# Optimization experiments

Hardware: AMD Instinct MI355X
Metric: run time of the kernel (lower is better)

## Reference

```python
import jax, jax.numpy as jnp
import numpy as np

KERNEL = 10   # kernel_size (asserted == 10 in the original)
HEADS = 4
BN_SCALE = 1.0 / np.sqrt(1.0 + 1e-5)  # eval-mode BatchNorm1d (running mean 0, var 1, affine 1/0)


def get_dct_matrix(N):
    k = np.arange(N)[:, None].astype(np.float64)
    i = np.arange(N)[None, :].astype(np.float64)
    w = np.full((N, 1), np.sqrt(2.0 / N))
    w[0, 0] = np.sqrt(1.0 / N)
    dct_m = w * np.cos(np.pi * (i + 0.5) * k / N)
    idct_m = np.linalg.inv(dct_m)
    return dct_m.astype(np.float32), idct_m.astype(np.float32)


def conv1d(x, w):  # x [B,C,L], w [O,I,K], valid, no bias
    return jax.lax.conv_general_dilated(x, w, (1,), 'VALID',
                                        dimension_numbers=('NCH', 'OIH', 'NCH'))


def conv_stack(x, w1, w2):  # Conv1d(k=6) -> ReLU -> Conv1d(k=5) -> ReLU
    return jax.nn.relu(conv1d(jax.nn.relu(conv1d(x, w1)), w2))


# vmap over the 4 heads' weights -> [H,B,D,L]
heads_conv = jax.vmap(conv_stack, in_axes=(None, 0, 0))


def _forward(src, cq1, cq2, ck1, ck2, lw, lb, giw, gia, gib, gbw, gba, gbb,
             gow, goa, gob, dct_n, output_n, input_n):
    bs, in_feat = src.shape[0], src.shape[2]
    src = src[:, :input_n]                                   # [B,50,48]
    src_key = jnp.swapaxes(src, 1, 2)[:, :, :input_n - output_n]  # [B,48,25]
    src_query = jnp.swapaxes(src, 1, 2)[:, :, -KERNEL:]           # [B,48,10]

    dct_np, idct_np = get_dct_matrix(KERNEL + output_n)
    dct_m = jnp.asarray(dct_np)
    idct_m = jnp.asarray(idct_np)

    vn = input_n - KERNEL - output_n + 1  # 16 overlapping value windows
    vl = KERNEL + output_n                # window length 35
    idx = np.arange(vl)[None, :] + np.arange(vn)[:, None]    # [16,35]
    windows = src[:, idx]                                    # [B,16,35,48]
    # DCT per window then flatten per-joint coeffs: [B,16,48*dct_n]
    val = jnp.einsum('dv,bnvf->bndf', dct_m[:dct_n], windows)
    src_value = jnp.swapaxes(val, 2, 3).reshape(bs, vn, -1)  # [B,16,480]

    key_h = heads_conv(src_key / 1000.0, ck1, ck2)           # [H,B,512,16]
    query_h = heads_conv(src_query / 1000.0, cq1, cq2)       # [H,B,512,1]

    # sum-normalized (non-softmax) attention
    score = jnp.einsum('hbdq,hbdk->hbqk', query_h, key_h) + 1e-15  # [H,B,1,16]
    att_w = score / jnp.sum(score, axis=3, keepdims=True)
    dct_att = jnp.einsum('hbk,bkf->hbf', att_w[:, :, 0], src_value)  # [H,B,480]
    dct_att = dct_att.reshape(HEADS, bs, in_feat, dct_n)
    att_cat = jnp.transpose(dct_att, (1, 0, 2, 3)).reshape(bs, HEADS * in_feat, dct_n)
    # Linear over the concatenated head/joint axis: [B,48,dct_n]
    att_lin = jnp.einsum('bmd,nm->bnd', att_cat, lw) + lb[None, :, None]

    # last kernel_size frames + last frame repeated output_n times
    gather_idx = np.concatenate([np.arange(input_n - KERNEL, input_n),
                                 np.full(output_n, input_n - 1)])
    input_gcn = src[:, gather_idx]                           # [B,35,48]
    dct_in = jnp.einsum('dv,bvf->bfd', dct_m[:dct_n], input_gcn)  # [B,48,10]
    dct_in = jnp.concatenate([dct_in, att_lin], axis=-1)     # [B,48,20]

    # GCN (Mao et al. style): learnable adjacency [48,48], eval-mode BN, tanh
    def gc(h, a, w, b):
        return jnp.einsum('nm,bmf->bnf', a, h @ w) + b

    y = jnp.tanh(gc(dct_in, gia, giw, gib) * BN_SCALE)       # [B,48,512]
    for s in range(gbw.shape[0]):
        r = y
        for j in range(2):
            y = jnp.tanh(gc(y, gba[s, j], gbw[s, j], gbb[s, j]) * BN_SCALE)
        y = y + r
    dct_out = gc(y, goa, gow, gob) + dct_in                  # [B,48,20]

    out_gcn = jnp.einsum('vd,bnd->bvn', idct_m[:, :dct_n], dct_out[:, :, :dct_n])  # [B,35,48]
    return out_gcn[:, :, None, :]                            # [B,35,itera=1,48]


def setup_inputs() -> dict:
    key = jax.random.key(0)
    ks = jax.random.split(key, 16)
    bs, in_feat, d_model, dct_n = 256, 48, 512, 10
    s = 0.05
    return {
        'src': jax.random.normal(ks[0], (bs, 50, in_feat), jnp.float32) * 1000.0,
        'convQ_w1': jax.random.normal(ks[1], (HEADS, d_model, in_feat, 6), jnp.float32) * s,
        'convQ_w2': jax.random.normal(ks[2], (HEADS, d_model, d_model, 5), jnp.float32) * s,
        'convK_w1': jax.random.normal(ks[3], (HEADS, d_model, in_feat, 6), jnp.float32) * s,
        'convK_w2': jax.random.normal(ks[4], (HEADS, d_model, d_model, 5), jnp.float32) * s,
        'linear_w': jax.random.normal(ks[5], (in_feat, HEADS * in_feat), jnp.float32) * s,
        'linear_b': jax.random.normal(ks[6], (in_feat,), jnp.float32) * s,
        'gc_in_w': jax.random.normal(ks[7], (2 * dct_n, d_model), jnp.float32) * s,
        'gc_in_att': jax.random.normal(ks[8], (in_feat, in_feat), jnp.float32) * s,
        'gc_in_b': jax.random.normal(ks[9], (d_model,), jnp.float32) * s,
        'gcb_w': jax.random.normal(ks[10], (2, 2, d_model, d_model), jnp.float32) * s,
        'gcb_att': jax.random.normal(ks[11], (2, 2, in_feat, in_feat), jnp.float32) * s,
        'gcb_b': jax.random.normal(ks[12], (2, 2, d_model), jnp.float32) * s,
        'gc_out_w': jax.random.normal(ks[13], (d_model, 2 * dct_n), jnp.float32) * s,
        'gc_out_att': jax.random.normal(ks[14], (in_feat, in_feat), jnp.float32) * s,
        'gc_out_b': jax.random.normal(ks[15], (2 * dct_n,), jnp.float32) * s,
        'dct_n': 10, 'output_n': 25, 'input_n': 50, 'itera': 1,
    }


def reference(src, convQ_w1, convQ_w2, convK_w1, convK_w2, linear_w, linear_b,
              gc_in_w, gc_in_att, gc_in_b, gcb_w, gcb_att, gcb_b,
              gc_out_w, gc_out_att, gc_out_b, dct_n, output_n, input_n, itera):
    # itera=1 path only (itera>1 in the original references undefined attrs)
    return _forward(src, convQ_w1, convQ_w2, convK_w1, convK_w2, linear_w, linear_b,
                    gc_in_w, gc_in_att, gc_in_b, gcb_w, gcb_att, gcb_b,
                    gc_out_w, gc_out_att, gc_out_b, dct_n, output_n, input_n)
```

## Files before the change

### kernel.cpp

```cpp
#include <hip/hip_runtime.h>
#include <math.h>

static constexpr float BN_SCALE_F = 0.9999950000374997f;

typedef __bf16 bf16;
typedef bf16 bf16x8 __attribute__((ext_vector_type(8)));
typedef bf16 bf16x4 __attribute__((ext_vector_type(4)));
typedef float floatx4 __attribute__((ext_vector_type(4)));

#define GLOBAL_AS __attribute__((address_space(1)))
#define LDS_AS __attribute__((address_space(3)))

enum { BM_SRC = 0, BM_R1K = 1, BM_PLAIN = 3 };

__device__ __forceinline__ float tanh_fast(float x) {
    const float e = __expf(2.f * x);
    return 1.f - 2.f / (e + 1.f);
}

__device__ __forceinline__ void d_trw1(int id, const float* w, bf16* wt) {
    if (id < 4 * 512 * 320) {
        int ho = id / 320, c = id % 320;
        float v = (c < 288) ? w[(long)ho * 288 + (c % 48) * 6 + (c / 48)] * 1e-3f : 0.f;
        wt[id] = (bf16)v;
    }
}
__global__ __launch_bounds__(256) void k_prep(
    const float* __restrict__ src, const float* __restrict__ cq1,
    const float* __restrict__ ck1, const float* __restrict__ cq2,
    const float* __restrict__ ck2, const float* __restrict__ gbw,
    const float* __restrict__ giw, const float* __restrict__ gow,
    const float* __restrict__ gba, float* __restrict__ dct10,
    bf16* __restrict__ srcbf, bf16* __restrict__ w1tq, bf16* __restrict__ w1tk,
    bf16* __restrict__ w2tq, bf16* __restrict__ w2tk, bf16* __restrict__ gbwt,
    bf16* __restrict__ giwP, bf16* __restrict__ gowT, bf16* __restrict__ gbaP) {
    __shared__ float lds[4160];
    int bb = blockIdx.x;
    const int t = threadIdx.x;
    if (bb < 2) {
        int id = bb * 256 + t;
        if (id < 350) {
            int k = id / 35, i = id % 35;
            double w = (k == 0) ? sqrt(1.0 / 35.0) : sqrt(2.0 / 35.0);
            dct10[id] = (float)(w * cos(3.14159265358979323846 * (i + 0.5) * k / 35.0));
        }
        return;
    }
    bb -= 2;
    if (bb < 2401) {
        int id = bb * 256 + t;
        if (id < 614656) srcbf[id] = (bf16)(id < 614400 ? src[id] : 0.f);
        return;
    }
    bb -= 2401;
    if (bb < 2560) { d_trw1(bb * 256 + t, cq1, w1tq); return; }
    bb -= 2560;
    if (bb < 2560) { d_trw1(bb * 256 + t, ck1, w1tk); return; }
    bb -= 2560;
    if (bb < 4096) {
        const bool isQ = bb < 2048;
        const int ho = isQ ? bb : bb - 2048;
        const float* wrow = (isQ ? cq2 : ck2) + (long)ho * 2560;
        bf16* orow = (isQ ? w2tq : w2tk) + (long)ho * 2560;
        for (int j = t; j < 2560; j += 256) lds[j] = wrow[j];
        __syncthreads();
        for (int c = t; c < 2560; c += 256) {
            const int k = c >> 9, ii = c & 511;
            orow[c] = (bf16)lds[ii * 5 + k];
        }
        return;
    }
    bb -= 4096;
    if (bb < 256) {
        const int s = bb >> 6, tile = bb & 63;
        const int tr = tile >> 3, tc = tile & 7;
        const float* in = gbw + (long)s * 262144;
        bf16* o = gbwt + (long)s * 262144;
#pragma unroll
        for (int r = 0; r < 16; ++r) {
            const int kl = (t >> 6) * 16 + r, ml = t & 63;
            lds[kl * 65 + ml] = in[(long)(tr * 64 + kl) * 512 + tc * 64 + ml];
        }
        __syncthreads();
#pragma unroll
        for (int r = 0; r < 16; ++r) {
            const int ml = (t >> 6) * 16 + r, kl = t & 63;
            o[(long)(tc * 64 + ml) * 512 + tr * 64 + kl] = (bf16)lds[kl * 65 + ml];
        }
        return;
    }
    bb -= 256;
    if (bb < 128) {
        int id = bb * 256 + t;
        if (id < 512 * 64) {
            int f = id >> 6, k = id & 63;
            giwP[id] = (bf16)(k < 20 ? giw[k * 512 + f] : 0.f);
        }
        return;
    }
    bb -= 128;
    if (bb < 64) {
        int id = bb * 256 + t;
        int d = id >> 9, k = id & 511;
        gowT[id] = (bf16)(d < 20 ? gow[k * 20 + d] : 0.f);
        return;
    }
    bb -= 64;
    {
        int id = bb * 256 + t;
        if (id < 12288) {
            int l = id / 3072, r = id % 3072, n = r >> 6, m = r & 63;
            gbaP[id] = (bf16)(m < 48 ? gba[l * 2304 + n * 48 + m] : 0.f);
        }
    }
}

struct GP {
    const bf16* A;
    const bf16* B;
    bf16* C;
    int NT;
    int toff;
    int nTiles;
    long aStr, bStr, cStr;
};
template <int BM1, int BM2>
__global__ __launch_bounds__(256) void mgemm2(GP p1, GP p2, const int splitX,
                                              const int M, const int K) {
    const bool first = (int)blockIdx.x < splitX;
    const GP p = first ? p1 : p2;
    const int bx = first ? (int)blockIdx.x : (int)blockIdx.x - splitX;
    if (bx >= p.nTiles) return;
    __shared__ bf16 As[128 * 64];
    __shared__ bf16 Bs[128 * 64];
    const int tid = threadIdx.x;
    const int wave = tid >> 6;
    const int lane = tid & 63;
    const int wm = (wave & 1) << 6;
    const int wn = (wave >> 1) << 6;
    const int m0 = blockIdx.y * 128;
    const int n0 = bx * 128;
    const bf16* A = p.A + (long)blockIdx.z * p.aStr;
    const bf16* B = p.B + (long)blockIdx.z * p.bStr;

    const int srow = lane >> 3;
    const int gch = (lane & 7) ^ srow;
    const bf16* aptr[4];
    const bf16* bptr[4];
#pragma unroll
    for (int i = 0; i < 4; ++i) {
        const int ar = wave * 32 + i * 8 + srow;
        aptr[i] = A + (long)(m0 + ar) * K + gch * 8;
        const int n = n0 + ar;
        long bbase;
        const bool isSrc = first ? (BM1 == BM_SRC) : (BM2 == BM_SRC);
        if (isSrc)
            bbase = (long)(n / p.NT) * 2400 + (long)((n % p.NT) + p.toff) * 48;
        else
            bbase = (long)n * K;
        bptr[i] = B + bbase + gch * 8;
    }
    const int ldsOff = wave * 32 * 64;

    floatx4 acc[4][4];
#pragma unroll
    for (int j = 0; j < 4; ++j)
#pragma unroll
        for (int i = 0; i < 4; ++i) acc[j][i] = (floatx4){0.f, 0.f, 0.f, 0.f};

    const int fr = lane & 15;
    const int fq = lane >> 4;
    const int fx = lane & 7;

    for (int k0 = 0; k0 < K; k0 += 64) {
#pragma unroll
        for (int i = 0; i < 4; ++i) {
            __builtin_amdgcn_global_load_lds(
                (const GLOBAL_AS void*)(aptr[i] + k0),
                (LDS_AS void*)(As + ldsOff + i * 512), 16, 0, 0);
            __builtin_amdgcn_global_load_lds(
                (const GLOBAL_AS void*)(bptr[i] + k0),
                (LDS_AS void*)(Bs + ldsOff + i * 512), 16, 0, 0);
        }
        __syncthreads();
#pragma unroll
        for (int kk = 0; kk < 2; ++kk) {
            bf16x8 af[4], bfr[4];
#pragma unroll
            for (int im = 0; im < 4; ++im)
                af[im] = *(const bf16x8*)(As + (wm + im * 16 + fr) * 64 +
                                          ((((kk << 2) + fq) ^ fx) << 3));
#pragma unroll
            for (int in = 0; in < 4; ++in)
                bfr[in] = *(const bf16x8*)(Bs + (wn + in * 16 + fr) * 64 +
                                           ((((kk << 2) + fq) ^ fx) << 3));
#pragma unroll
            for (int in = 0; in < 4; ++in)
#pragma unroll
                for (int im = 0; im < 4; ++im)
                    acc[in][im] = __builtin_amdgcn_mfma_f32_16x16x32_bf16(
                        af[im], bfr[in], acc[in][im], 0, 0, 0);
        }
        __syncthreads();
    }
#pragma unroll
    for (int in = 0; in < 4; ++in) {
        const long n = n0 + wn + in * 16 + fr;
#pragma unroll
        for (int im = 0; im < 4; ++im) {
            floatx4 v = acc[in][im];
            const long m = m0 + wm + im * 16 + (fq << 2);
            v.x = fmaxf(v.x, 0.f);
            v.y = fmaxf(v.y, 0.f);
            v.z = fmaxf(v.z, 0.f);
            v.w = fmaxf(v.w, 0.f);
            bf16* C = p.C + (long)blockIdx.z * p.cStr + n * M + m;
            bf16x4 ov;
            ov[0] = (bf16)v.x;
            ov[1] = (bf16)v.y;
            ov[2] = (bf16)v.z;
            ov[3] = (bf16)v.w;
            *(bf16x4*)C = ov;
        }
    }
}

__global__ __launch_bounds__(256) void k_conv2(
    const bf16* __restrict__ w2tk, const bf16* __restrict__ r1k,
    bf16* __restrict__ keyh, const bf16* __restrict__ w2tq,
    const bf16* __restrict__ r1q, bf16* __restrict__ qh) {
    const int M = 512, K = 2560;
    int bx, by, bz;
    const bf16 *A, *B;
    bf16* C;
    bool r1kMode;
    long aStr, bStr, cStr;
    {
        const int i = blockIdx.x;
        if (i < 512) {
            const int slot = i & 7;
            bz = slot & 3;
            const int half = slot >> 2;
            const int j = i >> 3;
            bx = half * 16 + (j & 15);
            by = j >> 4;
            A = w2tk; B = r1k; C = keyh; r1kMode = true;
            aStr = 512L * 2560; bStr = 2621440L; cStr = 2097152L;
        } else {
            const int j = i - 512;
            bx = j & 1;
            by = (j >> 1) & 3;
            bz = j >> 3;
            A = w2tq; B = r1q; C = qh; r1kMode = false;
            aStr = 512L * 2560; bStr = 655360L; cStr = 131072L;
        }
    }
    __shared__ bf16 As[128 * 64];
    __shared__ bf16 Bs[128 * 64];
    const int tid = threadIdx.x;
    const int wave = tid >> 6;
    const int lane = tid & 63;
    const int wm = (wave & 1) << 6;
    const int wn = (wave >> 1) << 6;
    const int m0 = by * 128;
    const int n0 = bx * 128;
    A += (long)bz * aStr;
    B += (long)bz * bStr;

    const int srow = lane >> 3;
    const int gch = (lane & 7) ^ srow;
    const bf16* aptr[4];
    const bf16* bptr[4];
#pragma unroll
    for (int i = 0; i < 4; ++i) {
        const int ar = wave * 32 + i * 8 + srow;
        aptr[i] = A + (long)(m0 + ar) * K + gch * 8;
        const int n = n0 + ar;
        const long bbase = r1kMode ? (long)((n >> 4) * 20 + (n & 15)) * 512
                                   : (long)n * K;
        bptr[i] = B + bbase + gch * 8;
    }
    const int ldsOff = wave * 32 * 64;

    floatx4 acc[4][4];
#pragma unroll
    for (int j = 0; j < 4; ++j)
#pragma unroll
        for (int i = 0; i < 4; ++i) acc[j][i] = (floatx4){0.f, 0.f, 0.f, 0.f};

    const int fr = lane & 15;
    const int fq = lane >> 4;
    const int fx = lane & 7;

    for (int k0 = 0; k0 < K; k0 += 64) {
#pragma unroll
        for (int i = 0; i < 4; ++i) {
            __builtin_amdgcn_global_load_lds(
                (const GLOBAL_AS void*)(aptr[i] + k0),
                (LDS_AS void*)(As + ldsOff + i * 512), 16, 0, 0);
            __builtin_amdgcn_global_load_lds(
                (const GLOBAL_AS void*)(bptr[i] + k0),
                (LDS_AS void*)(Bs + ldsOff + i * 512), 16, 0, 0);
        }
        __syncthreads();
#pragma unroll
        for (int kk = 0; kk < 2; ++kk) {
            bf16x8 af[4], bfr[4];
#pragma unroll
            for (int im = 0; im < 4; ++im)
                af[im] = *(const bf16x8*)(As + (wm + im * 16 + fr) * 64 +
                                          ((((kk << 2) + fq) ^ fx) << 3));
#pragma unroll
            for (int in = 0; in < 4; ++in)
                bfr[in] = *(const bf16x8*)(Bs + (wn + in * 16 + fr) * 64 +
                                           ((((kk << 2) + fq) ^ fx) << 3));
#pragma unroll
            for (int in = 0; in < 4; ++in)
#pragma unroll
                for (int im = 0; im < 4; ++im)
                    acc[in][im] = __builtin_amdgcn_mfma_f32_16x16x32_bf16(
                        af[im], bfr[in], acc[in][im], 0, 0, 0);
        }
        __syncthreads();
    }
#pragma unroll
    for (int in = 0; in < 4; ++in) {
        const long n = n0 + wn + in * 16 + fr;
#pragma unroll
        for (int im = 0; im < 4; ++im) {
            floatx4 v = acc[in][im];
            const long m = m0 + wm + im * 16 + (fq << 2);
            v.x = fmaxf(v.x, 0.f);
            v.y = fmaxf(v.y, 0.f);
            v.z = fmaxf(v.z, 0.f);
            v.w = fmaxf(v.w, 0.f);
            bf16* Cp = C + (long)bz * cStr + n * M + m;
            bf16x4 ov;
            ov[0] = (bf16)v.x;
            ov[1] = (bf16)v.y;
            ov[2] = (bf16)v.z;
            ov[3] = (bf16)v.w;
            *(bf16x4*)Cp = ov;
        }
    }
}

__global__ __launch_bounds__(512) void k_att(
    const bf16* __restrict__ qh, const bf16* __restrict__ keyh,
    const float* __restrict__ src, const float* __restrict__ dct10,
    const float* __restrict__ lw, const float* __restrict__ lb,
    const float* __restrict__ gia, float* __restrict__ dctin,
    bf16* __restrict__ z0) {
    const int b = blockIdx.x;
    const int t = threadIdx.x;
    __shared__ float BIG[9216];
    __shared__ float WD[2400];
    __shared__ float D[350];
    __shared__ float L[1920];
    __shared__ float dinS[960];
    __shared__ float sS[64];
    __shared__ float awS[64];

    {
        const int g = t >> 3, lane = t & 7;
        const int h = g >> 4, tt = g & 15;
        const bf16* q = qh + ((long)h * 256 + b) * 512 + lane * 64;
        const bf16* kr = keyh + (long)h * 2097152 + ((long)b * 16 + tt) * 512 + lane * 64;
        float p = 0.f;
#pragma unroll
        for (int i = 0; i < 8; ++i) {
            const bf16x8 qv = *(const bf16x8*)(q + i * 8);
            const bf16x8 kv = *(const bf16x8*)(kr + i * 8);
#pragma unroll
            for (int j = 0; j < 8; ++j) p = fmaf((float)qv[j], (float)kv[j], p);
        }
        p += __shfl_down(p, 4, 8);
        p += __shfl_down(p, 2, 8);
        p += __shfl_down(p, 1, 8);
        if (lane == 0) sS[g] = p + 1e-15f;
    }
    for (int i = t; i < 2400; i += 512) WD[i] = src[(long)b * 2400 + i];
    for (int i = t; i < 350; i += 512) D[i] = dct10[i];
    __syncthreads();
    if (t < 4) {
        float s = 0.f;
#pragma unroll
        for (int k = 0; k < 16; ++k) s += sS[t * 16 + k];
        const float inv = 1.f / s;
#pragma unroll
        for (int k = 0; k < 16; ++k) awS[t * 16 + k] = sS[t * 16 + k] * inv;
    }
    __syncthreads();
    if (t < 480) {
        const int f = t / 10, d = t % 10;
        float dreg[35];
#pragma unroll
        for (int v = 0; v < 35; ++v) dreg[v] = D[d * 35 + v];
#pragma unroll 2
        for (int n = 0; n < 16; ++n) {
            float acc = 0.f;
#pragma unroll
            for (int v = 0; v < 35; ++v)
                acc = fmaf(dreg[v], WD[(n + v) * 48 + f], acc);
            BIG[n * 480 + t] = acc;
        }
        float acc = 0.f;
#pragma unroll
        for (int v = 0; v < 10; ++v)
            acc = fmaf(dreg[v], WD[(40 + v) * 48 + f], acc);
        float cs = 0.f;
#pragma unroll
        for (int v = 10; v < 35; ++v) cs += dreg[v];
        acc = fmaf(cs, WD[49 * 48 + f], acc);
        dinS[f * 20 + d] = acc;
        dctin[(long)b * 960 + f * 20 + d] = acc;
    }
    __syncthreads();
    for (int p = 0; p < 4; ++p) {
        const int idx = t + p * 512;
        if (idx < 1920) {
            const int h = idx / 480, j = idx % 480;
            float acc = 0.f;
#pragma unroll
            for (int k = 0; k < 16; ++k)
                acc = fmaf(awS[h * 16 + k], BIG[k * 480 + j], acc);
            L[idx] = acc;
        }
    }
    __syncthreads();
    for (int i = t; i < 9216; i += 512) BIG[i] = lw[i];
    for (int i = t; i < 2304; i += 512) WD[i] = gia[i];
    __syncthreads();
    if (t < 480) {
        const int n = t / 10, d = t % 10;
        float acc = lb[n];
#pragma unroll
        for (int h = 0; h < 4; ++h)
#pragma unroll
            for (int f = 0; f < 48; ++f)
                acc = fmaf(BIG[n * 192 + h * 48 + f], L[h * 480 + f * 10 + d], acc);
        dinS[n * 20 + 10 + d] = acc;
        dctin[(long)b * 960 + n * 20 + 10 + d] = acc;
    }
    __syncthreads();
    for (int p = 0; p < 2; ++p) {
        const int idx = t + p * 512;
        if (idx < 960) {
            const int n = idx / 20, d = idx % 20;
            float acc = 0.f;
#pragma unroll
            for (int m = 0; m < 48; ++m)
                acc = fmaf(WD[n * 48 + m], dinS[m * 20 + d], acc);
            z0[((long)b * 48 + n) * 64 + d] = (bf16)acc;
        }
    }
    for (int i = t; i < 2112; i += 512) {
        const int n = i / 44, c = 20 + i % 44;
        z0[((long)b * 48 + n) * 64 + c] = (bf16)0.f;
    }
}

template <bool TOUT>
__device__ __forceinline__ void gcn_matmul2(
    const bf16* __restrict__ zSrc, const bf16* __restrict__ Bg, const int K,
    const float* __restrict__ bias, const bf16* __restrict__ resT,
    bf16* __restrict__ outS, const int wave, const int lane) {
    const int fr = lane & 15, fq = lane >> 4;
    const int f0 = wave * 32;
    floatx4 acc[3][2];
#pragma unroll
    for (int it = 0; it < 3; ++it)
#pragma unroll
        for (int jt = 0; jt < 2; ++jt) acc[it][jt] = (floatx4){0.f, 0.f, 0.f, 0.f};
    const bf16* bp0 = Bg + (long)(f0 + fr) * K + fq * 8;
    const bf16* bp1 = bp0 + 16 * (long)K;
    bf16x8 a0 = *(const bf16x8*)(bp0);
    bf16x8 a1 = *(const bf16x8*)(bp1);
    bf16x8 b0 = *(const bf16x8*)(bp0 + 32);
    bf16x8 b1 = *(const bf16x8*)(bp1 + 32);
    for (int k0 = 0; k0 < K; k0 += 64) {
        bf16x8 p0 = a0, p1 = a1, q0 = b0, q1 = b1;
        if (k0 + 64 < K) {
            p0 = *(const bf16x8*)(bp0 + k0 + 64);
            p1 = *(const bf16x8*)(bp1 + k0 + 64);
            q0 = *(const bf16x8*)(bp0 + k0 + 96);
            q1 = *(const bf16x8*)(bp1 + k0 + 96);
        }
        bf16x8 af[3];
#pragma unroll
        for (int it = 0; it < 3; ++it)
            af[it] = *(const bf16x8*)(zSrc + (it * 16 + fr) * 520 + k0 + fq * 8);
#pragma unroll
        for (int it = 0; it < 3; ++it) {
            acc[it][0] = __builtin_amdgcn_mfma_f32_16x16x32_bf16(af[it], a0,
                                                                acc[it][0], 0, 0, 0);
            acc[it][1] = __builtin_amdgcn_mfma_f32_16x16x32_bf16(af[it], a1,
                                                                acc[it][1], 0, 0, 0);
        }
#pragma unroll
        for (int it = 0; it < 3; ++it)
            af[it] = *(const bf16x8*)(zSrc + (it * 16 + fr) * 520 + k0 + 32 + fq * 8);
#pragma unroll
        for (int it = 0; it < 3; ++it) {
            acc[it][0] = __builtin_amdgcn_mfma_f32_16x16x32_bf16(af[it], b0,
                                                                acc[it][0], 0, 0, 0);
            acc[it][1] = __builtin_amdgcn_mfma_f32_16x16x32_bf16(af[it], b1,
                                                                acc[it][1], 0, 0, 0);
        }
        a0 = p0; a1 = p1; b0 = q0; b1 = q1;
    }
#pragma unroll
    for (int jt = 0; jt < 2; ++jt) {
        const int f = f0 + jt * 16 + fr;
        const float bv = bias[f];
#pragma unroll
        for (int it = 0; it < 3; ++it)
#pragma unroll
            for (int r = 0; r < 4; ++r) {
                const int irow = it * 16 + fq * 4 + r;
                float v = tanh_fast((acc[it][jt][r] + bv) * BN_SCALE_F);
                if (resT) v += (float)resT[f * 48 + irow];
                if (TOUT)
                    outS[f * 48 + irow] = (bf16)v;
                else
                    outS[irow * 520 + f] = (bf16)v;
            }
    }
}

__device__ __forceinline__ void gcn_attmul2(const bf16* __restrict__ gA,
                                            const bf16* __restrict__ YinT,
                                            bf16* __restrict__ zOut,
                                            const int wave, const int lane) {
    const int fr = lane & 15, fq = lane >> 4;
    const int f0 = wave * 32;
    floatx4 acc[3][2];
#pragma unroll
    for (int it = 0; it < 3; ++it)
#pragma unroll
        for (int jt = 0; jt < 2; ++jt) acc[it][jt] = (floatx4){0.f, 0.f, 0.f, 0.f};
    bf16x8 af0[3], af1[3], bv0[2], bv1[2];
#pragma unroll
    for (int it = 0; it < 3; ++it) {
        af0[it] = *(const bf16x8*)(gA + (it * 16 + fr) * 64 + fq * 8);
        af1[it] = *(const bf16x8*)(gA + (it * 16 + fr) * 64 + 32 + fq * 8);
    }
#pragma unroll
    for (int jt = 0; jt < 2; ++jt) {
        const int f = f0 + jt * 16 + fr;
        bv0[jt] = *(const bf16x8*)(YinT + f * 48 + fq * 8);
        bv1[jt] = *(const bf16x8*)(YinT + f * 48 + 32 + fq * 8);
    }
#pragma unroll
    for (int it = 0; it < 3; ++it)
#pragma unroll
        for (int jt = 0; jt < 2; ++jt) {
            acc[it][jt] = __builtin_amdgcn_mfma_f32_16x16x32_bf16(af0[it], bv0[jt],
                                                                 acc[it][jt], 0, 0, 0);
            acc[it][jt] = __builtin_amdgcn_mfma_f32_16x16x32_bf16(af1[it], bv1[jt],
                                                                 acc[it][jt], 0, 0, 0);
        }
#pragma unroll
    for (int jt = 0; jt < 2; ++jt) {
        const int f = f0 + jt * 16 + fr;
#pragma unroll
        for (int it = 0; it < 3; ++it)
#pragma unroll
            for (int r = 0; r < 4; ++r)
                zOut[(it * 16 + fq * 4 + r) * 520 + f] = (bf16)acc[it][jt][r];
    }
}

__global__ __launch_bounds__(1024) void k_gcn(
    const bf16* __restrict__ z0, const bf16* __restrict__ giwP,
    const float* __restrict__ gib, const bf16* __restrict__ gbwt,
    const bf16* __restrict__ gbaP, const float* __restrict__ gbb,
    const float* __restrict__ goa, const bf16* __restrict__ gowT,
    const float* __restrict__ gob, const float* __restrict__ dctin,
    const float* __restrict__ dct10, float* __restrict__ out) {
    const int b = blockIdx.x;
    const int t = threadIdx.x;
    const int wave = t >> 6, lane = t & 63;
    __shared__ __align__(16) bf16 yaS[24976];
    __shared__ __align__(16) bf16 ybS[24592];
    __shared__ __align__(16) bf16 zS[48 * 520];

    if (t < 384) {
        const int r = t >> 3, c = t & 7;
        *(bf16x8*)(zS + r * 520 + c * 8) =
            *(const bf16x8*)(z0 + ((long)b * 48 + r) * 64 + c * 8);
    } else if (t < 400) {
        yaS[24576 + (t - 384)] = (bf16)0.f;
    } else if (t < 416) {
        ybS[24576 + (t - 400)] = (bf16)0.f;
    }
    __syncthreads();
    gcn_matmul2<true>(zS, giwP, 64, gib, nullptr, yaS, wave, lane);
    __syncthreads();

#pragma unroll
    for (int l = 0; l < 4; ++l) {
        const bf16* YinT = (l == 0 || l == 3) ? yaS : ybS;
        gcn_attmul2(gbaP + l * 3072, YinT, zS, wave, lane);
        __syncthreads();
        const bf16* Res = (l == 1) ? yaS : (l == 3 ? ybS : nullptr);
        if (l < 3)
            gcn_matmul2<true>(zS, gbwt + (long)l * 262144, 512, gbb + l * 512,
                              Res, (l < 2) ? ybS : yaS, wave, lane);
        else
            gcn_matmul2<false>(zS, gbwt + 3L * 262144, 512, gbb + 3 * 512, Res,
                               yaS, wave, lane);
        __syncthreads();
    }
    float* T2 = (float*)ybS;
    float* dS = ((float*)ybS) + 960;
    float* goaS = ((float*)ybS) + 1920;
    float* Df = ((float*)ybS) + 4224;
    if (t < 384) {
        const int fr2 = lane & 15, fq2 = lane >> 4;
        const int it = wave >> 1, jt = wave & 1;
        floatx4 accT = (floatx4){0.f, 0.f, 0.f, 0.f};
        const bf16* ap = yaS + (it * 16 + fr2) * 520 + fq2 * 8;
        const bf16* gp = gowT + (long)(jt * 16 + fr2) * 512 + fq2 * 8;
        for (int k0 = 0; k0 < 512; k0 += 32) {
            const bf16x8 av = *(const bf16x8*)(ap + k0);
            const bf16x8 gv = *(const bf16x8*)(gp + k0);
            accT = __builtin_amdgcn_mfma_f32_16x16x32_bf16(av, gv, accT, 0, 0, 0);
        }
        const int d = jt * 16 + fr2;
        if (d < 20) {
#pragma unroll
            for (int r = 0; r < 4; ++r) {
                const int m = it * 16 + fq2 * 4 + r;
                T2[m * 20 + d] = accT[r];
            }
        }
    } else {
        for (int i = t - 384; i < 2304; i += 640) goaS[i] = goa[i];
        for (int i = t - 384; i < 350; i += 640) Df[i] = dct10[i];
    }
    __syncthreads();
    if (t < 960) {
        const int n = t / 20, d = t % 20;
        float acc = gob[d] + dctin[(long)b * 960 + t];
#pragma unroll
        for (int m = 0; m < 48; ++m)
            acc = fmaf(goaS[n * 48 + m], T2[m * 20 + d], acc);
        dS[t] = acc;
    }
    __syncthreads();
    for (int e = t; e < 1680; e += 1024) {
        const int v = e / 48, n = e % 48;
        float acc = 0.f;
#pragma unroll
        for (int d = 0; d < 10; ++d)
            acc = fmaf(Df[d * 35 + v], dS[n * 20 + d], acc);
        out[(long)b * 1680 + e] = acc;
    }
}

static constexpr size_t WS_DCT10 = 0;
static constexpr size_t WS_ATTW = 1536;
static constexpr size_t WS_QH = WS_ATTW + 65536;
static constexpr size_t WS_DCTIN = WS_QH + 2097152;
static constexpr size_t WS_DCTOUT = WS_DCTIN + 983040;
static constexpr size_t WS_SRCVAL = WS_DCTOUT + 983040;
static constexpr size_t WS_PAD0 = WS_SRCVAL + 7864320;
static constexpr size_t WS_GOWT = WS_PAD0;
static constexpr size_t WS_GBAP = WS_PAD0 + 32768;
static constexpr size_t WS_SRCBF = WS_PAD0 + 8388608;
static constexpr size_t WS_W1TQ = WS_SRCBF + 1229824;
static constexpr size_t WS_W1TK = WS_W1TQ + 1310720;
static constexpr size_t WS_W2TQ = WS_W1TK + 1310720;
static constexpr size_t WS_W2TK = WS_W2TQ + 10485760;
static constexpr size_t WS_GBWT = WS_W2TK + 10485760;
static constexpr size_t WS_R1K = WS_GBWT + 2097152;
static constexpr size_t WS_R1Q = WS_R1K + 20971520;
static constexpr size_t WS_T = WS_R1Q + 5242880;
static constexpr size_t WS_GIWP = WS_T + 50331648;
static constexpr size_t WS_KEYH = WS_T;
static constexpr size_t WS_Z0 = WS_T + 17825792;

extern "C" void kernel_launch(void* const* d_in, const int* in_sizes, int n_in,
                              void* d_out, int out_size, void* d_ws,
                              size_t ws_size, hipStream_t stream) {
    const float* src = (const float*)d_in[0];
    const float* cq1 = (const float*)d_in[1];
    const float* cq2 = (const float*)d_in[2];
    const float* ck1 = (const float*)d_in[3];
    const float* ck2 = (const float*)d_in[4];
    const float* lw = (const float*)d_in[5];
    const float* lb = (const float*)d_in[6];
    const float* giw = (const float*)d_in[7];
    const float* gia = (const float*)d_in[8];
    const float* gib = (const float*)d_in[9];
    const float* gbw = (const float*)d_in[10];
    const float* gba = (const float*)d_in[11];
    const float* gbb = (const float*)d_in[12];
    const float* gow = (const float*)d_in[13];
    const float* goa = (const float*)d_in[14];
    const float* gob = (const float*)d_in[15];
    float* out = (float*)d_out;
    char* ws = (char*)d_ws;

    float* dct10 = (float*)(ws + WS_DCT10);
    bf16* qh = (bf16*)(ws + WS_QH);
    float* dctin = (float*)(ws + WS_DCTIN);
    bf16* keyh = (bf16*)(ws + WS_KEYH);
    bf16* srcbf = (bf16*)(ws + WS_SRCBF);
    bf16* w1tq = (bf16*)(ws + WS_W1TQ);
    bf16* w1tk = (bf16*)(ws + WS_W1TK);
    bf16* w2tq = (bf16*)(ws + WS_W2TQ);
    bf16* w2tk = (bf16*)(ws + WS_W2TK);
    bf16* gbwt = (bf16*)(ws + WS_GBWT);
    bf16* r1k = (bf16*)(ws + WS_R1K);
    bf16* r1q = (bf16*)(ws + WS_R1Q);
    bf16* giwP = (bf16*)(ws + WS_GIWP);
    bf16* gowT = (bf16*)(ws + WS_GOWT);
    bf16* gbaP = (bf16*)(ws + WS_GBAP);
    bf16* z0 = (bf16*)(ws + WS_Z0);

    k_prep<<<12115, 256, 0, stream>>>(src, cq1, ck1, cq2, ck2, gbw, giw, gow,
                                      gba, dct10, srcbf, w1tq, w1tk, w2tq,
                                      w2tk, gbwt, giwP, gowT, gbaP);

    {
        GP pk{w1tk, srcbf, r1k, 20, 0, 40, 512L * 320, 0L, 5120L * 512};
        GP pq{w1tq, srcbf, r1q, 5, 40, 10, 512L * 320, 0L, 1280L * 512};
        mgemm2<BM_SRC, BM_SRC><<<dim3(56, 4, 4), 256, 0, stream>>>(pk, pq, 40,
                                                                   512, 320);
    }
    k_conv2<<<544, 256, 0, stream>>>(w2tk, r1k, keyh, w2tq, r1q, qh);

    k_att<<<256, 512, 0, stream>>>(qh, keyh, src, dct10, lw, lb, gia, dctin, z0);

    k_gcn<<<256, 1024, 0, stream>>>(z0, giwP, gib, gbwt, gbaP, gbb, goa, gowT,
                                    gob, dctin, dct10, out);
}
```

Measured before the change: 355.2 us.

## Pre-swizzle GCN weights into MFMA fragment order and deepen prefetch pipeline

The prep kernel now writes the GCN block weights and input weights in a per-wave, per-k-step fragment layout, so each lane in the GCN matmul reads one contiguous 16-byte chunk per fragment and the wave's reads are fully coalesced. The matmul is rewritten with a compile-time step count, a fully unrolled k loop and a three-deep rotating register prefetch of weight fragments. The epilogue also switches residual reads and transposed-output writes to 4-wide bf16 vectors. In exchange it uses more registers for the prefetch buffers and adds index arithmetic to the one-time weight preparation.

Result: faster. 334.1 us (-5.9%).

```diff
diff --git a/kernel.cpp b/kernel.cpp
--- a/kernel.cpp
+++ b/kernel.cpp
@@ -32,8 +32,8 @@
     const float* __restrict__ giw, const float* __restrict__ gow,
     const float* __restrict__ gba, float* __restrict__ dct10,
     bf16* __restrict__ srcbf, bf16* __restrict__ w1tq, bf16* __restrict__ w1tk,
-    bf16* __restrict__ w2tq, bf16* __restrict__ w2tk, bf16* __restrict__ gbwt,
-    bf16* __restrict__ giwP, bf16* __restrict__ gowT, bf16* __restrict__ gbaP) {
+    bf16* __restrict__ w2tq, bf16* __restrict__ w2tk, bf16* __restrict__ gbwF,
+    bf16* __restrict__ giwF, bf16* __restrict__ gowT, bf16* __restrict__ gbaP) {
     __shared__ float lds[4160];
     int bb = blockIdx.x;
     const int t = threadIdx.x;
@@ -72,29 +72,41 @@
     }
     bb -= 4096;
     if (bb < 256) {
-        const int s = bb >> 6, tile = bb & 63;
+        const int l = bb >> 6, tile = bb & 63;
         const int tr = tile >> 3, tc = tile & 7;
-        const float* in = gbw + (long)s * 262144;
-        bf16* o = gbwt + (long)s * 262144;
+        const float* in = gbw + (long)l * 262144;
+        bf16* o = gbwF + (long)l * 262144;
 #pragma unroll
         for (int r = 0; r < 16; ++r) {
             const int kl = (t >> 6) * 16 + r, ml = t & 63;
             lds[kl * 65 + ml] = in[(long)(tr * 64 + kl) * 512 + tc * 64 + ml];
         }
         __syncthreads();
-#pragma unroll
-        for (int r = 0; r < 16; ++r) {
-            const int ml = (t >> 6) * 16 + r, kl = t & 63;
-            o[(long)(tc * 64 + ml) * 512 + tr * 64 + kl] = (bf16)lds[kl * 65 + ml];
+        for (int j = t; j < 4096; j += 256) {
+            const int q = j >> 9, r4 = j & 511;
+            const int gl = q >> 2, sl = (q >> 1) & 1, jt = q & 1;
+            const int lane = r4 >> 3, e = r4 & 7;
+            const int fr = lane & 15, fq = lane >> 4;
+            const int kk = sl * 32 + fq * 8 + e;
+            const int ff = gl * 32 + jt * 16 + fr;
+            o[(long)(tc * 2 + gl) * 16384 + (long)(tr * 2 + sl) * 1024 + jt * 512 + r4] =
+                (bf16)lds[kk * 65 + ff];
         }
         return;
     }
     bb -= 256;
     if (bb < 128) {
         int id = bb * 256 + t;
-        if (id < 512 * 64) {
-            int f = id >> 6, k = id & 63;
-            giwP[id] = (bf16)(k < 20 ? giw[k * 512 + f] : 0.f);
+        if (id < 32768) {
+            const int r2 = id & 2047;
+            const int s = r2 >> 10, r3 = r2 & 1023;
+            const int jt = r3 >> 9, r4 = r3 & 511;
+            const int lane = r4 >> 3, e = r4 & 7;
+            const int fr = lane & 15, fq = lane >> 4;
+            const int g = id >> 11;
+            const int k = s * 32 + fq * 8 + e;
+            const int f = g * 32 + jt * 16 + fr;
+            giwF[id] = (bf16)(k < 20 ? giw[k * 512 + f] : 0.f);
         }
         return;
     }
@@ -460,9 +472,9 @@
     }
 }
 
-template <bool TOUT>
-__device__ __forceinline__ void gcn_matmul2(
-    const bf16* __restrict__ zSrc, const bf16* __restrict__ Bg, const int K,
+template <bool TOUT, int S>
+__device__ __forceinline__ void gcn_matmul3(
+    const bf16* __restrict__ zSrc, const bf16* __restrict__ Wf,
     const float* __restrict__ bias, const bf16* __restrict__ resT,
     bf16* __restrict__ outS, const int wave, const int lane) {
     const int fr = lane & 15, fq = lane >> 4;
@@ -472,59 +484,61 @@
     for (int it = 0; it < 3; ++it)
 #pragma unroll
         for (int jt = 0; jt < 2; ++jt) acc[it][jt] = (floatx4){0.f, 0.f, 0.f, 0.f};
-    const bf16* bp0 = Bg + (long)(f0 + fr) * K + fq * 8;
-    const bf16* bp1 = bp0 + 16 * (long)K;
-    bf16x8 a0 = *(const bf16x8*)(bp0);
-    bf16x8 a1 = *(const bf16x8*)(bp1);
-    bf16x8 b0 = *(const bf16x8*)(bp0 + 32);
-    bf16x8 b1 = *(const bf16x8*)(bp1 + 32);
-    for (int k0 = 0; k0 < K; k0 += 64) {
-        bf16x8 p0 = a0, p1 = a1, q0 = b0, q1 = b1;
-        if (k0 + 64 < K) {
-            p0 = *(const bf16x8*)(bp0 + k0 + 64);
-            p1 = *(const bf16x8*)(bp1 + k0 + 64);
-            q0 = *(const bf16x8*)(bp0 + k0 + 96);
-            q1 = *(const bf16x8*)(bp1 + k0 + 96);
-        }
+    const bf16* wp = Wf + (long)wave * (S * 1024) + (lane << 3);
+    bf16x8 w0[4], w1[4];
+    constexpr int PRE = (S < 3) ? S : 3;
+#pragma unroll
+    for (int s = 0; s < PRE; ++s) {
+        w0[s] = *(const bf16x8*)(wp + s * 1024);
+        w1[s] = *(const bf16x8*)(wp + s * 1024 + 512);
+    }
+#pragma unroll
+    for (int s = 0; s < S; ++s) {
         bf16x8 af[3];
 #pragma unroll
         for (int it = 0; it < 3; ++it)
-            af[it] = *(const bf16x8*)(zSrc + (it * 16 + fr) * 520 + k0 + fq * 8);
+            af[it] = *(const bf16x8*)(zSrc + (it * 16 + fr) * 520 + s * 32 + fq * 8);
+        if (s + 3 < S) {
+            const int ns = (s + 3) & 3;
+            w0[ns] = *(const bf16x8*)(wp + (s + 3) * 1024);
+            w1[ns] = *(const bf16x8*)(wp + (s + 3) * 1024 + 512);
+        }
+        const int sl = s & 3;
 #pragma unroll
         for (int it = 0; it < 3; ++it) {
-            acc[it][0] = __builtin_amdgcn_mfma_f32_16x16x32_bf16(af[it], a0,
+            acc[it][0] = __builtin_amdgcn_mfma_f32_16x16x32_bf16(af[it], w0[sl],
                                                                 acc[it][0], 0, 0, 0);
-            acc[it][1] = __builtin_amdgcn_mfma_f32_16x16x32_bf16(af[it], a1,
+            acc[it][1] = __builtin_amdgcn_mfma_f32_16x16x32_bf16(af[it], w1[sl],
                                                                 acc[it][1], 0, 0, 0);
         }
-#pragma unroll
-        for (int it = 0; it < 3; ++it)
-            af[it] = *(const bf16x8*)(zSrc + (it * 16 + fr) * 520 + k0 + 32 + fq * 8);
-#pragma unroll
-        for (int it = 0; it < 3; ++it) {
-            acc[it][0] = __builtin_amdgcn_mfma_f32_16x16x32_bf16(af[it], b0,
-                                                                acc[it][0], 0, 0, 0);
-            acc[it][1] = __builtin_amdgcn_mfma_f32_16x16x32_bf16(af[it], b1,
-                                                                acc[it][1], 0, 0, 0);
-        }
-        a0 = p0; a1 = p1; b0 = q0; b1 = q1;
     }
 #pragma unroll
     for (int jt = 0; jt < 2; ++jt) {
         const int f = f0 + jt * 16 + fr;
         const float bv = bias[f];
 #pragma unroll
-        for (int it = 0; it < 3; ++it)
-#pragma unroll
-            for (int r = 0; r < 4; ++r) {
-                const int irow = it * 16 + fq * 4 + r;
-                float v = tanh_fast((acc[it][jt][r] + bv) * BN_SCALE_F);
-                if (resT) v += (float)resT[f * 48 + irow];
-                if (TOUT)
-                    outS[f * 48 + irow] = (bf16)v;
-                else
-                    outS[irow * 520 + f] = (bf16)v;
+        for (int it = 0; it < 3; ++it) {
+            const int ir0 = it * 16 + fq * 4;
+            float v[4];
+#pragma unroll
+            for (int r = 0; r < 4; ++r)
+                v[r] = tanh_fast((acc[it][jt][r] + bv) * BN_SCALE_F);
+            if (resT) {
+                const bf16x4 rv = *(const bf16x4*)(resT + f * 48 + ir0);
+#pragma unroll
+                for (int r = 0; r < 4; ++r) v[r] += (float)rv[r];
             }
+            if (TOUT) {
+                bf16x4 ov;
+#pragma unroll
+                for (int r = 0; r < 4; ++r) ov[r] = (bf16)v[r];
+                *(bf16x4*)(outS + f * 48 + ir0) = ov;
+            } else {
+#pragma unroll
+                for (int r = 0; r < 4; ++r)
+                    outS[(ir0 + r) * 520 + f] = (bf16)v[r];
+            }
+        }
     }
 }
 
@@ -572,8 +586,8 @@
 }
 
 __global__ __launch_bounds__(1024) void k_gcn(
-    const bf16* __restrict__ z0, const bf16* __restrict__ giwP,
-    const float* __restrict__ gib, const bf16* __restrict__ gbwt,
+    const bf16* __restrict__ z0, const bf16* __restrict__ giwF,
+    const float* __restrict__ gib, const bf16* __restrict__ gbwF,
     const bf16* __restrict__ gbaP, const float* __restrict__ gbb,
     const float* __restrict__ goa, const bf16* __restrict__ gowT,
     const float* __restrict__ gob, const float* __restrict__ dctin,
@@ -595,7 +609,7 @@
         ybS[24576 + (t - 400)] = (bf16)0.f;
     }
     __syncthreads();
-    gcn_matmul2<true>(zS, giwP, 64, gib, nullptr, yaS, wave, lane);
+    gcn_matmul3<true, 2>(zS, giwF, gib, nullptr, yaS, wave, lane);
     __syncthreads();
 
 #pragma unroll
@@ -605,11 +619,11 @@
         __syncthreads();
         const bf16* Res = (l == 1) ? yaS : (l == 3 ? ybS : nullptr);
         if (l < 3)
-            gcn_matmul2<true>(zS, gbwt + (long)l * 262144, 512, gbb + l * 512,
-                              Res, (l < 2) ? ybS : yaS, wave, lane);
+            gcn_matmul3<true, 16>(zS, gbwF + (long)l * 262144, gbb + l * 512,
+                                  Res, (l < 2) ? ybS : yaS, wave, lane);
         else
-            gcn_matmul2<false>(zS, gbwt + 3L * 262144, 512, gbb + 3 * 512, Res,
-                               yaS, wave, lane);
+            gcn_matmul3<false, 16>(zS, gbwF + 3L * 262144, gbb + 3 * 512, Res,
+                                   yaS, wave, lane);
         __syncthreads();
     }
     float* T2 = (float*)ybS;
@@ -712,17 +726,17 @@
     bf16* w1tk = (bf16*)(ws + WS_W1TK);
     bf16* w2tq = (bf16*)(ws + WS_W2TQ);
     bf16* w2tk = (bf16*)(ws + WS_W2TK);
-    bf16* gbwt = (bf16*)(ws + WS_GBWT);
+    bf16* gbwF = (bf16*)(ws + WS_GBWT);
     bf16* r1k = (bf16*)(ws + WS_R1K);
     bf16* r1q = (bf16*)(ws + WS_R1Q);
-    bf16* giwP = (bf16*)(ws + WS_GIWP);
+    bf16* giwF = (bf16*)(ws + WS_GIWP);
     bf16* gowT = (bf16*)(ws + WS_GOWT);
     bf16* gbaP = (bf16*)(ws + WS_GBAP);
     bf16* z0 = (bf16*)(ws + WS_Z0);
 
     k_prep<<<12115, 256, 0, stream>>>(src, cq1, ck1, cq2, ck2, gbw, giw, gow,
                                       gba, dct10, srcbf, w1tq, w1tk, w2tq,
-                                      w2tk, gbwt, giwP, gowT, gbaP);
+                                      w2tk, gbwF, giwF, gowT, gbaP);
 
     {
         GP pk{w1tk, srcbf, r1k, 20, 0, 40, 512L * 320, 0L, 5120L * 512};
@@ -734,6 +748,6 @@
 
     k_att<<<256, 512, 0, stream>>>(qh, keyh, src, dct10, lw, lb, gia, dctin, z0);
 
-    k_gcn<<<256, 1024, 0, stream>>>(z0, giwP, gib, gbwt, gbaP, gbb, goa, gowT,
+    k_gcn<<<256, 1024, 0, stream>>>(z0, giwF, gib, gbwF, gbaP, gbb, goa, gowT,
                                     gob, dctin, dct10, out);
 }
```
